# Kernel optimization log

Hardware: AMD Instinct MI355X
Metric: run time of the kernel (lower is better)

Reference implementation:

```python
import jax, jax.numpy as jnp
import numpy as np

N_NODES = 50000
N_EDGES = 800000


def setup_inputs() -> dict:
    key = jax.random.key(0)
    ks = jax.random.split(key, 9)
    d, h, hd = 128, 4, 32
    s = 1.0 / np.sqrt(d)
    return {
        "x": jax.random.normal(ks[0], (N_NODES, d), jnp.float32),
        "edge_index": jax.random.randint(ks[1], (2, N_EDGES), 0, N_NODES, jnp.int32),
        "W0": jax.random.normal(ks[2], (d, d), jnp.float32) * s,
        "att_l0": jax.random.normal(ks[3], (h, hd), jnp.float32) * s,
        "att_r0": jax.random.normal(ks[4], (h, hd), jnp.float32) * s,
        "b0": jnp.zeros((d,), jnp.float32),
        "W1": jax.random.normal(ks[5], (d, d), jnp.float32) * s,
        "att_l1": jax.random.normal(ks[6], (h, hd), jnp.float32) * s,
        "att_r1": jax.random.normal(ks[7], (h, hd), jnp.float32) * s,
        "b1": jnp.zeros((hd,), jnp.float32),
    }


def _gat_layer(x, src, dst, W, att_l, att_r, bias, concat):
    # x: [N, F_in]; W: [H*D, F_in] (torch Linear layout); att_*: [H, D]
    n = x.shape[0]
    h, d = att_l.shape
    hx = (x @ W.T).reshape(n, h, d)                     # [N,H,D]
    al = jnp.einsum('nhd,hd->nh', hx, att_l)            # [N,H]
    ar = jnp.einsum('nhd,hd->nh', hx, att_r)
    att = al[src] + ar[dst]                             # [E,H]
    att = jax.nn.leaky_relu(att, negative_slope=0.2)
    # segment softmax over destination nodes
    m = jax.ops.segment_max(att, dst, num_segments=n)   # [N,H]
    att = jnp.exp(att - m[dst])
    ssum = jax.ops.segment_sum(att, dst, num_segments=n)
    att = att / (ssum[dst] + 1e-9)                      # [E,H]
    msgs = att[:, :, None] * hx[src]                    # [E,H,D]
    out = jax.ops.segment_sum(msgs, dst, num_segments=n)  # [N,H,D]
    if concat:
        out = out.reshape(n, h * d)
    else:
        out = out.mean(axis=1)
    return out + bias


def reference(x, edge_index, W0, att_l0, att_r0, b0, W1, att_l1, att_r1, b1):
    src, dst = edge_index[0], edge_index[1]
    x = _gat_layer(x, src, dst, W0, att_l0, att_r0, b0, concat=True)
    x = jax.nn.relu(x)  # dropout is identity in eval mode
    x = _gat_layer(x, src, dst, W1, att_l1, att_r1, b1, concat=False)
    return x
```

## Files before the change

### kernel.cpp

```cpp
#include <hip/hip_runtime.h>
#include <hip/hip_bf16.h>

#define H 4
#define D 32
#define F 128
#define MAXDEG 64
#define PF 8
#define NBUCK 256
#define BUCKW 196
#define NABLK 128
#define SEGCAP 64
#define GB    1563
#define HXP   136
#define SIS   68

typedef __attribute__((ext_vector_type(8))) short bf16x8;
typedef __attribute__((ext_vector_type(4))) float f32x4;

__device__ __forceinline__ short f2bf(float v) {
    __hip_bfloat16 h = __float2bfloat16(v);
    return *reinterpret_cast<short*>(&h);
}
__device__ __forceinline__ float bf2f(short s) {
    __hip_bfloat16 h = *reinterpret_cast<__hip_bfloat16*>(&s);
    return __bfloat162float(h);
}

__device__ __forceinline__
void wconv_part(int part8, const float* __restrict__ W0, short* __restrict__ W0hi,
                short* __restrict__ W0lo, const float* __restrict__ W1,
                short* __restrict__ W1hi, short* __restrict__ W1lo) {
    const int tid = threadIdx.x;
    const float* W  = (part8 < 4) ? W0 : W1;
    short* Whi = (part8 < 4) ? W0hi : W1hi;
    short* Wlo = (part8 < 4) ? W0lo : W1lo;
    const int part = part8 & 3;
    const int base = part * (F * F / 4);
    for (int i = base + tid * 4; i < base + F * F / 4; i += 1024) {
        float4 v = *reinterpret_cast<const float4*>(W + i);
        float vv[4] = {v.x, v.y, v.z, v.w};
        short hs[4], ls[4];
#pragma unroll
        for (int j = 0; j < 4; ++j) {
            hs[j] = f2bf(vv[j]);
            ls[j] = f2bf(vv[j] - bf2f(hs[j]));
        }
        *reinterpret_cast<short4*>(Whi + i) = make_short4(hs[0], hs[1], hs[2], hs[3]);
        *reinterpret_cast<short4*>(Wlo + i) = make_short4(ls[0], ls[1], ls[2], ls[3]);
    }
}

__device__ __forceinline__
void bucketA_body(int abid, const int* __restrict__ ei, int E,
                  int* __restrict__ cntmat, unsigned int* __restrict__ buf) {
    __shared__ int lcnt[NBUCK];
    const int tid = threadIdx.x;
    lcnt[tid] = 0;
    __syncthreads();
    const int per = ((E / NABLK) + 3) & ~3;
    const int e0 = abid * per;
    const int e1 = min(e0 + per, E);
    for (int e = e0 + 4 * tid; e < e1; e += 1024) {
        int4 dv = *reinterpret_cast<const int4*>(ei + E + e);
        atomicAdd(&lcnt[dv.x / BUCKW], 1);
        atomicAdd(&lcnt[dv.y / BUCKW], 1);
        atomicAdd(&lcnt[dv.z / BUCKW], 1);
        atomicAdd(&lcnt[dv.w / BUCKW], 1);
    }
    __syncthreads();
    cntmat[abid * NBUCK + tid] = min(lcnt[tid], SEGCAP);
    lcnt[tid] = 0;
    __syncthreads();
    for (int e = e0 + 4 * tid; e < e1; e += 1024) {
        int4 sv = *reinterpret_cast<const int4*>(ei + e);
        int4 dv = *reinterpret_cast<const int4*>(ei + E + e);
        int ss[4] = {sv.x, sv.y, sv.z, sv.w};
        int dd[4] = {dv.x, dv.y, dv.z, dv.w};
#pragma unroll
        for (int j = 0; j < 4; ++j) {
            int b = dd[j] / BUCKW;
            int pos = atomicAdd(&lcnt[b], 1);
            if (pos < SEGCAP)
                buf[((size_t)b * NABLK + abid) * SEGCAP + pos] =
                    (unsigned)ss[j] | ((unsigned)(dd[j] - b * BUCKW) << 16);
        }
    }
}

__global__ __launch_bounds__(256)
void k_init(const int* __restrict__ ei, int E, int* __restrict__ cntmat,
            unsigned int* __restrict__ buf,
            const float* __restrict__ W0, short* __restrict__ W0hi,
            short* __restrict__ W0lo, const float* __restrict__ W1,
            short* __restrict__ W1hi, short* __restrict__ W1lo) {
    const int bid = blockIdx.x;
    if (bid < NABLK)
        bucketA_body(bid, ei, E, cntmat, buf);
    else
        wconv_part(bid - NABLK, W0, W0hi, W0lo, W1, W1hi, W1lo);
}

__device__ __forceinline__
void bucketB_body(int b, const unsigned int* __restrict__ buf,
                  const int* __restrict__ cntmat, int* __restrict__ deg,
                  unsigned short* __restrict__ ssrc2u, int N,
                  int* cnt, int* scnt, unsigned short* slots) {
    const int tid = threadIdx.x;
    if (tid < BUCKW) cnt[tid] = 0;
    if (tid < NABLK) scnt[tid] = cntmat[tid * NBUCK + b];
    __syncthreads();
    const int a    = tid & (NABLK - 1);
    const int half = tid >> 7;
    const int mm   = scnt[a];
    const unsigned int* seg = buf + ((size_t)b * NABLK + a) * SEGCAP;
    for (int c = half * 4; c < mm; c += 8) {
        uint4 r = *reinterpret_cast<const uint4*>(seg + c);
        unsigned rr[4] = {r.x, r.y, r.z, r.w};
#pragma unroll
        for (int j = 0; j < 4; ++j) {
            if (c + j < mm) {
                int src  = rr[j] & 0xffff;
                int ldst = rr[j] >> 16;
                int slot = atomicAdd(&cnt[ldst], 1);
                if (slot < MAXDEG)
                    slots[ldst * MAXDEG + slot] = (unsigned short)src;
            }
        }
    }
    __syncthreads();
    uint4* dst = reinterpret_cast<uint4*>(ssrc2u + (size_t)b * BUCKW * MAXDEG);
    const uint4* s4 = reinterpret_cast<const uint4*>(slots);
    for (int i = tid; i < BUCKW * MAXDEG / 8; i += 256)
        dst[i] = s4[i];
    if (tid < BUCKW) {
        int node = b * BUCKW + tid;
        if (node < N) deg[node] = cnt[tid];
    }
}

__device__ __forceinline__
void bsetup_pre(const short* __restrict__ Whi, const short* __restrict__ Wlo,
                int wave, int m, int q8, bf16x8 Bhi[2][4], bf16x8 Blo[2][4]) {
#pragma unroll
    for (int j = 0; j < 2; ++j) {
        const int fout = wave * 32 + j * 16 + m;
#pragma unroll
        for (int kc = 0; kc < 4; ++kc) {
            Bhi[j][kc] = *reinterpret_cast<const bf16x8*>(Whi + (size_t)fout * F + kc * 32 + q8);
            Blo[j][kc] = *reinterpret_cast<const bf16x8*>(Wlo + (size_t)fout * F + kc * 32 + q8);
        }
    }
}

__device__ __forceinline__
void loadA_f32(const float* __restrict__ X, int node0, int m, int q8, float4 r[8]) {
    const float* xp = X + (size_t)(node0 + m) * F + q8;
#pragma unroll
    for (int kc = 0; kc < 4; ++kc) {
        r[2 * kc]     = *reinterpret_cast<const float4*>(xp + kc * 32);
        r[2 * kc + 1] = *reinterpret_cast<const float4*>(xp + kc * 32 + 4);
    }
}

__device__ __forceinline__
void splitA(const float4 r[8], bf16x8 Ahi[4], bf16x8 Alo[4]) {
#pragma unroll
    for (int kc = 0; kc < 4; ++kc) {
        float xv[8] = {r[2 * kc].x, r[2 * kc].y, r[2 * kc].z, r[2 * kc].w,
                       r[2 * kc + 1].x, r[2 * kc + 1].y, r[2 * kc + 1].z, r[2 * kc + 1].w};
#pragma unroll
        for (int t2 = 0; t2 < 8; ++t2) {
            short hh = f2bf(xv[t2]);
            Ahi[kc][t2] = hh;
            Alo[kc][t2] = f2bf(xv[t2] - bf2f(hh));
        }
    }
}

__device__ __forceinline__
void mfma_epi(int tile, const bf16x8 Ahi[4], const bf16x8 Alo[4],
              const bf16x8 Bhi[2][4], const bf16x8 Blo[2][4],
              float alw0, float alw16, float arw0, float arw16,
              short* hxs, float* __restrict__ AL,
              float* __restrict__ AR, int wave, int m, int q) {
    const int node0 = tile * 16;
    f32x4 acc0 = {0.f, 0.f, 0.f, 0.f};
    f32x4 acc1 = {0.f, 0.f, 0.f, 0.f};
#pragma unroll
    for (int kc = 0; kc < 4; ++kc) {
        acc0 = __builtin_amdgcn_mfma_f32_16x16x32_bf16(Ahi[kc], Bhi[0][kc], acc0, 0, 0, 0);
        acc1 = __builtin_amdgcn_mfma_f32_16x16x32_bf16(Ahi[kc], Bhi[1][kc], acc1, 0, 0, 0);
        acc0 = __builtin_amdgcn_mfma_f32_16x16x32_bf16(Ahi[kc], Blo[0][kc], acc0, 0, 0, 0);
        acc1 = __builtin_amdgcn_mfma_f32_16x16x32_bf16(Ahi[kc], Blo[1][kc], acc1, 0, 0, 0);
        acc0 = __builtin_amdgcn_mfma_f32_16x16x32_bf16(Alo[kc], Bhi[0][kc], acc0, 0, 0, 0);
        acc1 = __builtin_amdgcn_mfma_f32_16x16x32_bf16(Alo[kc], Bhi[1][kc], acc1, 0, 0, 0);
    }
    const int row0 = node0 + q * 4;
    const int col0 = wave * 32 + m;
#pragma unroll
    for (int r = 0; r < 4; ++r) {
        hxs[(q * 4 + r) * HXP + col0]      = f2bf(acc0[r]);
        hxs[(q * 4 + r) * HXP + col0 + 16] = f2bf(acc1[r]);
        float pal = acc0[r] * alw0 + acc1[r] * alw16;
        float par = acc0[r] * arw0 + acc1[r] * arw16;
#pragma unroll
        for (int o = 1; o < 16; o <<= 1) {
            pal += __shfl_xor(pal, o);
            par += __shfl_xor(par, o);
        }
        if (m == 0) {
            AL[(size_t)(row0 + r) * H + wave] = pal;
            AR[(size_t)(row0 + r) * H + wave] = par;
        }
    }
}

__device__ __forceinline__
void hxb_writeout(const short* hxs, int tile, __hip_bfloat16* __restrict__ HXB) {
    const int tid = threadIdx.x;
    const int row = tid >> 4;
    const int col = (tid & 15) * 8;
    uint4 v = *reinterpret_cast<const uint4*>(hxs + row * HXP + col);
    *reinterpret_cast<uint4*>(reinterpret_cast<short*>(HXB) +
                              (size_t)(tile * 16 + row) * F + col) = v;
}

__device__ __forceinline__
void gemm_pair_f32(int bid, const float* __restrict__ X,
                   const short* __restrict__ Whi, const short* __restrict__ Wlo,
                   const float* __restrict__ attl, const float* __restrict__ attr,
                   __hip_bfloat16* __restrict__ HXB, float* __restrict__ AL,
                   float* __restrict__ AR, int ntiles, short* hxs) {
    const int wave = threadIdx.x >> 6;
    const int lane = threadIdx.x & 63;
    const int m    = lane & 15;
    const int q    = lane >> 4;
    const int q8   = q * 8;
    bf16x8 Bhi[2][4], Blo[2][4];
    bsetup_pre(Whi, Wlo, wave, m, q8, Bhi, Blo);
    const float alw0  = attl[wave * 32 + m];
    const float alw16 = attl[wave * 32 + 16 + m];
    const float arw0  = attr[wave * 32 + m];
    const float arw16 = attr[wave * 32 + 16 + m];

    const int t0 = bid, t1 = bid + GB;
    const bool has1 = t1 < ntiles;
    float4 r0[8], r1[8];
    loadA_f32(X, t0 * 16, m, q8, r0);
    if (has1) loadA_f32(X, t1 * 16, m, q8, r1);
    bf16x8 Ahi[4], Alo[4];
    splitA(r0, Ahi, Alo);
    mfma_epi(t0, Ahi, Alo, Bhi, Blo, alw0, alw16, arw0, arw16, hxs, AL, AR, wave, m, q);
    if (has1) {
        splitA(r1, Ahi, Alo);
        mfma_epi(t1, Ahi, Alo, Bhi, Blo, alw0, alw16, arw0, arw16,
                 hxs + 16 * HXP, AL, AR, wave, m, q);
    }
    __syncthreads();
    hxb_writeout(hxs, t0, HXB);
    if (has1) hxb_writeout(hxs + 16 * HXP, t1, HXB);
}

__global__ __launch_bounds__(256)
void k_mid(const unsigned int* __restrict__ buf, const int* __restrict__ cntmat,
           int* __restrict__ deg, unsigned short* __restrict__ ssrc2u, int N,
           const float* __restrict__ X, const short* __restrict__ W0hi,
           const short* __restrict__ W0lo, const float* __restrict__ attl0,
           const float* __restrict__ attr0, __hip_bfloat16* __restrict__ HXB,
           float* __restrict__ AL, float* __restrict__ AR, int ntiles) {
    __shared__ union {
        struct {
            int cnt[BUCKW];
            int scnt[NABLK];
            unsigned short slots[BUCKW * MAXDEG];
        } bb;
        short hxs[2 * 16 * HXP];
    } sm;
    const int bid = blockIdx.x;
    if (bid < NBUCK)
        bucketB_body(bid, buf, cntmat, deg, ssrc2u, N,
                     sm.bb.cnt, sm.bb.scnt, sm.bb.slots);
    else
        gemm_pair_f32(bid - NBUCK, X, W0hi, W0lo, attl0, attr0, HXB, AL, AR,
                      ntiles, sm.hxs);
}

__device__ __forceinline__
int2 stage_idx16(int g, int lt, int n, const unsigned short* __restrict__ ssrc2u,
                 const int* __restrict__ deg, unsigned short* sidx) {
    const int cnt  = min(deg[n], MAXDEG);
    const int rcnt = (cnt + PF - 1) & ~(PF - 1);
    for (int t2 = lt; t2 < rcnt; t2 += 16)
        sidx[g * SIS + t2] =
            (t2 < cnt) ? ssrc2u[(size_t)n * MAXDEG + t2] : (unsigned short)0;
    __builtin_amdgcn_wave_barrier();
    return make_int2(cnt, rcnt);
}

__device__ __forceinline__
void gather16(int g, int lt, int cnt, int rcnt,
              const __hip_bfloat16* __restrict__ HXB,
              const float* __restrict__ AL, float ar_h,
              const unsigned short* sidx, float a[8], float& wsum) {
    const int h = lt >> 2;
    const unsigned short* hx = reinterpret_cast<const unsigned short*>(HXB);
    for (int base = 0; base < rcnt; base += PF) {
        uint4 v[PF];
        float alv[PF];
#pragma unroll
        for (int j = 0; j < PF; ++j) {
            int s = sidx[g * SIS + base + j];
            v[j]   = *reinterpret_cast<const uint4*>(hx + (size_t)s * F + 8 * lt);
            alv[j] = AL[s * H + h];
        }
#pragma unroll
        for (int j = 0; j < PF; ++j) {
            float t = alv[j] + ar_h;
            t = t > 0.f ? t : 0.2f * t;
            float w = (base + j < cnt) ? __expf(t) : 0.f;
            unsigned ww[4] = {v[j].x, v[j].y, v[j].z, v[j].w};
#pragma unroll
            for (int k = 0; k < 4; ++k) {
                a[2 * k]     += w * bf2f((short)(ww[k] & 0xffff));
                a[2 * k + 1] += w * bf2f((short)(ww[k] >> 16));
            }
            wsum += w;
        }
    }
}

__global__ __launch_bounds__(256)
void k_ag1(const unsigned short* __restrict__ ssrc2u, const int* __restrict__ deg,
           const float* __restrict__ AL0, const float* __restrict__ AR0,
           const __hip_bfloat16* __restrict__ HXB0, const float* __restrict__ b0,
           const short* __restrict__ W1hi, const short* __restrict__ W1lo,
           const float* __restrict__ attl1, const float* __restrict__ attr1,
           __hip_bfloat16* __restrict__ HXB1, float* __restrict__ AL1,
           float* __restrict__ AR1, int ntiles) {
    __shared__ union {
        unsigned short sidx[16 * SIS];
        short hxs[16 * HXP];
    } u;
    __shared__ short x1h[16 * HXP];
    __shared__ short x1l[16 * HXP];
    const int tid  = threadIdx.x;
    const int g    = tid >> 4;
    const int lt   = tid & 15;
    const int tile = blockIdx.x;

    {
        const int n = tile * 16 + g;
        const int h = lt >> 2;
        const float ar_h = AR0[(size_t)n * H + h];
        int2 cr = stage_idx16(g, lt, n, ssrc2u, deg, u.sidx);
        float a[8] = {0.f, 0.f, 0.f, 0.f, 0.f, 0.f, 0.f, 0.f};
        float ws = 0.f;
        gather16(g, lt, cr.x, cr.y, HXB0, AL0, ar_h, u.sidx, a, ws);
        float inv = 1.f / (ws + 1e-9f);
        const float4 b4a = *reinterpret_cast<const float4*>(b0 + 8 * lt);
        const float4 b4b = *reinterpret_cast<const float4*>(b0 + 8 * lt + 4);
        float bb[8] = {b4a.x, b4a.y, b4a.z, b4a.w, b4b.x, b4b.y, b4b.z, b4b.w};
        unsigned hw[4], lw[4];
#pragma unroll
        for (int k = 0; k < 4; ++k) {
            float o0 = fmaxf(a[2 * k] * inv + bb[2 * k], 0.f);
            float o1 = fmaxf(a[2 * k + 1] * inv + bb[2 * k + 1], 0.f);
            short h0 = f2bf(o0), h1 = f2bf(o1);
            short l0 = f2bf(o0 - bf2f(h0)), l1 = f2bf(o1 - bf2f(h1));
            hw[k] = (unsigned)(unsigned short)h0 | ((unsigned)(unsigned short)h1 << 16);
            lw[k] = (unsigned)(unsigned short)l0 | ((unsigned)(unsigned short)l1 << 16);
        }
        uint4 hv = {hw[0], hw[1], hw[2], hw[3]};
        uint4 lv = {lw[0], lw[1], lw[2], lw[3]};
        *reinterpret_cast<uint4*>(x1h + g * HXP + 8 * lt) = hv;
        *reinterpret_cast<uint4*>(x1l + g * HXP + 8 * lt) = lv;
    }
    __syncthreads();

    {
        const int wave = tid >> 6;
        const int lane = tid & 63;
        const int m    = lane & 15;
        const int q    = lane >> 4;
        const int q8   = q * 8;
        bf16x8 Bhi[2][4], Blo[2][4];
        bsetup_pre(W1hi, W1lo, wave, m, q8, Bhi, Blo);
        const float alw0  = attl1[wave * 32 + m];
        const float alw16 = attl1[wave * 32 + 16 + m];
        const float arw0  = attr1[wave * 32 + m];
        const float arw16 = attr1[wave * 32 + 16 + m];
        bf16x8 Ahi[4], Alo[4];
#pragma unroll
        for (int kc = 0; kc < 4; ++kc) {
            Ahi[kc] = *reinterpret_cast<const bf16x8*>(x1h + m * HXP + kc * 32 + q8);
            Alo[kc] = *reinterpret_cast<const bf16x8*>(x1l + m * HXP + kc * 32 + q8);
        }
        mfma_epi(tile, Ahi, Alo, Bhi, Blo, alw0, alw16, arw0, arw16,
                 u.hxs, AL1, AR1, wave, m, q);
    }
    __syncthreads();
    hxb_writeout(u.hxs, tile, HXB1);
}

__global__ __launch_bounds__(256)
void k_aggr1(const unsigned short* __restrict__ ssrc2u, const int* __restrict__ deg,
             const float* __restrict__ AL, const float* __restrict__ AR,
             const __hip_bfloat16* __restrict__ HXB, const float* __restrict__ bias,
             float* __restrict__ out, int N) {
    __shared__ unsigned short sidx[16 * SIS];
    const int tid = threadIdx.x;
    const int g   = tid >> 4;
    const int lt  = tid & 15;
    const int n   = blockIdx.x * 16 + g;
    const int h   = lt >> 2;
    const float ar_h = AR[(size_t)n * H + h];
    int2 cr = stage_idx16(g, lt, n, ssrc2u, deg, sidx);
    float a[8] = {0.f, 0.f, 0.f, 0.f, 0.f, 0.f, 0.f, 0.f};
    float ws = 0.f;
    gather16(g, lt, cr.x, cr.y, HXB, AL, ar_h, sidx, a, ws);
    float inv = 1.f / (ws + 1e-9f);
    float v[8];
#pragma unroll
    for (int k = 0; k < 8; ++k) {
        v[k] = a[k] * inv;
        v[k] += __shfl_xor(v[k], 4);
        v[k] += __shfl_xor(v[k], 8);
    }
    if (lt < 4) {
        const float4 b4a = *reinterpret_cast<const float4*>(bias + 8 * lt);
        const float4 b4b = *reinterpret_cast<const float4*>(bias + 8 * lt + 4);
        float4 o0, o1;
        o0.x = 0.25f * v[0] + b4a.x;
        o0.y = 0.25f * v[1] + b4a.y;
        o0.z = 0.25f * v[2] + b4a.z;
        o0.w = 0.25f * v[3] + b4a.w;
        o1.x = 0.25f * v[4] + b4b.x;
        o1.y = 0.25f * v[5] + b4b.y;
        o1.z = 0.25f * v[6] + b4b.z;
        o1.w = 0.25f * v[7] + b4b.w;
        *reinterpret_cast<float4*>(out + (size_t)n * D + 8 * lt)     = o0;
        *reinterpret_cast<float4*>(out + (size_t)n * D + 8 * lt + 4) = o1;
    }
}

extern "C" void kernel_launch(void* const* d_in, const int* in_sizes, int n_in,
                              void* d_out, int out_size, void* d_ws, size_t ws_size,
                              hipStream_t stream) {
    const float* x     = (const float*)d_in[0];
    const int*   ei    = (const int*)d_in[1];
    const float* W0    = (const float*)d_in[2];
    const float* attl0 = (const float*)d_in[3];
    const float* attr0 = (const float*)d_in[4];
    const float* b0    = (const float*)d_in[5];
    const float* W1    = (const float*)d_in[6];
    const float* attl1 = (const float*)d_in[7];
    const float* attr1 = (const float*)d_in[8];
    const float* b1    = (const float*)d_in[9];

    const int N = in_sizes[0] / F;
    const int E = in_sizes[1] / 2;
    const int ntiles = N / 16;

    char* p = (char*)d_ws;
    __hip_bfloat16* HXB0 = (__hip_bfloat16*)p; p += (size_t)N * F * 2;
    __hip_bfloat16* HXB1 = (__hip_bfloat16*)p; p += (size_t)N * F * 2;
    short* W0hi = (short*)p;                   p += (size_t)F * F * 2;
    short* W0lo = (short*)p;                   p += (size_t)F * F * 2;
    short* W1hi = (short*)p;                   p += (size_t)F * F * 2;
    short* W1lo = (short*)p;                   p += (size_t)F * F * 2;
    float* AL0  = (float*)p;                   p += (size_t)N * H * 4;
    float* AR0  = (float*)p;                   p += (size_t)N * H * 4;
    float* AL1  = (float*)p;                   p += (size_t)N * H * 4;
    float* AR1  = (float*)p;                   p += (size_t)N * H * 4;
    unsigned short* ssrc2u = (unsigned short*)p;
    p += (size_t)NBUCK * BUCKW * MAXDEG * 2;
    int* deg = (int*)p;                        p += (size_t)N * 4;
    unsigned int* buf = (unsigned int*)p;      p += (size_t)NBUCK * NABLK * SEGCAP * 4;
    int* cntmat = (int*)p;

    k_init<<<NABLK + 8, 256, 0, stream>>>(ei, E, cntmat, buf,
                                          W0, W0hi, W0lo, W1, W1hi, W1lo);

    k_mid<<<NBUCK + GB, 256, 0, stream>>>(buf, cntmat, deg, ssrc2u, N,
                                          x, W0hi, W0lo, attl0, attr0,
                                          HXB0, AL0, AR0, ntiles);

    k_ag1<<<ntiles, 256, 0, stream>>>(ssrc2u, deg, AL0, AR0, HXB0, b0,
                                      W1hi, W1lo, attl1, attr1,
                                      HXB1, AL1, AR1, ntiles);

    k_aggr1<<<ntiles, 256, 0, stream>>>(ssrc2u, deg, AL1, AR1, HXB1, b1,
                                        (float*)d_out, N);
}
```

Measured before the change: 204.0 us.

## Sort nodes by degree within buckets to balance layer-1 aggregation tiles

Each bucket block now builds a degree histogram and a per-bucket permutation that groups nodes of similar in-degree. The first aggregation-plus-GEMM kernel processes nodes in this permuted order, so the 16 node groups in a tile have similar trip counts and less warp divergence and tail imbalance. Results are scattered back to their original rows through the rowids indirection, with padding nodes masked out. This adds a scan step, a serial prefix sum on one thread per bucket, scattered output writes and extra tiles to cover the padded node range.

```diff
diff --git a/kernel.cpp b/kernel.cpp
--- a/kernel.cpp
+++ b/kernel.cpp
@@ -8,6 +8,7 @@
 #define PF 8
 #define NBUCK 256
 #define BUCKW 196
+#define NPAD  (NBUCK * BUCKW)
 #define NABLK 128
 #define SEGCAP 64
 #define GB    1563
@@ -103,11 +104,12 @@
 __device__ __forceinline__
 void bucketB_body(int b, const unsigned int* __restrict__ buf,
                   const int* __restrict__ cntmat, int* __restrict__ deg,
-                  unsigned short* __restrict__ ssrc2u, int N,
-                  int* cnt, int* scnt, unsigned short* slots) {
+                  unsigned short* __restrict__ ssrc2u, int* __restrict__ perm,
+                  int N, int* cnt, int* scnt, int* dh, unsigned short* slots) {
     const int tid = threadIdx.x;
     if (tid < BUCKW) cnt[tid] = 0;
     if (tid < NABLK) scnt[tid] = cntmat[tid * NBUCK + b];
+    if (tid <= MAXDEG) dh[tid] = 0;
     __syncthreads();
     const int a    = tid & (NABLK - 1);
     const int half = tid >> 7;
@@ -132,9 +134,22 @@
     const uint4* s4 = reinterpret_cast<const uint4*>(slots);
     for (int i = tid; i < BUCKW * MAXDEG / 8; i += 256)
         dst[i] = s4[i];
+    int d = 0;
     if (tid < BUCKW) {
         int node = b * BUCKW + tid;
+        d = min(cnt[tid], MAXDEG);
         if (node < N) deg[node] = cnt[tid];
+        atomicAdd(&dh[d], 1);
+    }
+    __syncthreads();
+    if (tid == 0) {
+        int acc = 0;
+        for (int i = 0; i <= MAXDEG; ++i) { int c = dh[i]; dh[i] = acc; acc += c; }
+    }
+    __syncthreads();
+    if (tid < BUCKW) {
+        int r = atomicAdd(&dh[d], 1);
+        perm[b * BUCKW + r] = b * BUCKW + tid;
     }
 }
 
@@ -178,12 +193,12 @@
 }
 
 __device__ __forceinline__
-void mfma_epi(int tile, const bf16x8 Ahi[4], const bf16x8 Alo[4],
+void mfma_epi(int node0, const int* rowids, int Nlim,
+              const bf16x8 Ahi[4], const bf16x8 Alo[4],
               const bf16x8 Bhi[2][4], const bf16x8 Blo[2][4],
               float alw0, float alw16, float arw0, float arw16,
               short* hxs, float* __restrict__ AL,
               float* __restrict__ AR, int wave, int m, int q) {
-    const int node0 = tile * 16;
     f32x4 acc0 = {0.f, 0.f, 0.f, 0.f};
     f32x4 acc1 = {0.f, 0.f, 0.f, 0.f};
 #pragma unroll
@@ -195,7 +210,6 @@
         acc0 = __builtin_amdgcn_mfma_f32_16x16x32_bf16(Alo[kc], Bhi[0][kc], acc0, 0, 0, 0);
         acc1 = __builtin_amdgcn_mfma_f32_16x16x32_bf16(Alo[kc], Bhi[1][kc], acc1, 0, 0, 0);
     }
-    const int row0 = node0 + q * 4;
     const int col0 = wave * 32 + m;
 #pragma unroll
     for (int r = 0; r < 4; ++r) {
@@ -209,20 +223,27 @@
             par += __shfl_xor(par, o);
         }
         if (m == 0) {
-            AL[(size_t)(row0 + r) * H + wave] = pal;
-            AR[(size_t)(row0 + r) * H + wave] = par;
-        }
-    }
-}
-
-__device__ __forceinline__
-void hxb_writeout(const short* hxs, int tile, __hip_bfloat16* __restrict__ HXB) {
+            int rid = rowids ? rowids[q * 4 + r] : (node0 + q * 4 + r);
+            if (rid < Nlim) {
+                AL[(size_t)rid * H + wave] = pal;
+                AR[(size_t)rid * H + wave] = par;
+            }
+        }
+    }
+}
+
+__device__ __forceinline__
+void hxb_writeout(const short* hxs, int node0, const int* rowids, int Nlim,
+                  __hip_bfloat16* __restrict__ HXB) {
     const int tid = threadIdx.x;
     const int row = tid >> 4;
     const int col = (tid & 15) * 8;
-    uint4 v = *reinterpret_cast<const uint4*>(hxs + row * HXP + col);
-    *reinterpret_cast<uint4*>(reinterpret_cast<short*>(HXB) +
-                              (size_t)(tile * 16 + row) * F + col) = v;
+    int node = rowids ? rowids[row] : (node0 + row);
+    if (node < Nlim) {
+        uint4 v = *reinterpret_cast<const uint4*>(hxs + row * HXP + col);
+        *reinterpret_cast<uint4*>(reinterpret_cast<short*>(HXB) +
+                                  (size_t)node * F + col) = v;
+    }
 }
 
 __device__ __forceinline__
@@ -250,20 +271,22 @@
     if (has1) loadA_f32(X, t1 * 16, m, q8, r1);
     bf16x8 Ahi[4], Alo[4];
     splitA(r0, Ahi, Alo);
-    mfma_epi(t0, Ahi, Alo, Bhi, Blo, alw0, alw16, arw0, arw16, hxs, AL, AR, wave, m, q);
+    mfma_epi(t0 * 16, nullptr, 1 << 30, Ahi, Alo, Bhi, Blo,
+             alw0, alw16, arw0, arw16, hxs, AL, AR, wave, m, q);
     if (has1) {
         splitA(r1, Ahi, Alo);
-        mfma_epi(t1, Ahi, Alo, Bhi, Blo, alw0, alw16, arw0, arw16,
-                 hxs + 16 * HXP, AL, AR, wave, m, q);
-    }
-    __syncthreads();
-    hxb_writeout(hxs, t0, HXB);
-    if (has1) hxb_writeout(hxs + 16 * HXP, t1, HXB);
+        mfma_epi(t1 * 16, nullptr, 1 << 30, Ahi, Alo, Bhi, Blo,
+                 alw0, alw16, arw0, arw16, hxs + 16 * HXP, AL, AR, wave, m, q);
+    }
+    __syncthreads();
+    hxb_writeout(hxs, t0 * 16, nullptr, 1 << 30, HXB);
+    if (has1) hxb_writeout(hxs + 16 * HXP, t1 * 16, nullptr, 1 << 30, HXB);
 }
 
 __global__ __launch_bounds__(256)
 void k_mid(const unsigned int* __restrict__ buf, const int* __restrict__ cntmat,
-           int* __restrict__ deg, unsigned short* __restrict__ ssrc2u, int N,
+           int* __restrict__ deg, unsigned short* __restrict__ ssrc2u,
+           int* __restrict__ perm, int N,
            const float* __restrict__ X, const short* __restrict__ W0hi,
            const short* __restrict__ W0lo, const float* __restrict__ attl0,
            const float* __restrict__ attr0, __hip_bfloat16* __restrict__ HXB,
@@ -272,23 +295,25 @@
         struct {
             int cnt[BUCKW];
             int scnt[NABLK];
+            int dh[MAXDEG + 1];
             unsigned short slots[BUCKW * MAXDEG];
         } bb;
         short hxs[2 * 16 * HXP];
     } sm;
     const int bid = blockIdx.x;
     if (bid < NBUCK)
-        bucketB_body(bid, buf, cntmat, deg, ssrc2u, N,
-                     sm.bb.cnt, sm.bb.scnt, sm.bb.slots);
+        bucketB_body(bid, buf, cntmat, deg, ssrc2u, perm, N,
+                     sm.bb.cnt, sm.bb.scnt, sm.bb.dh, sm.bb.slots);
     else
         gemm_pair_f32(bid - NBUCK, X, W0hi, W0lo, attl0, attr0, HXB, AL, AR,
                       ntiles, sm.hxs);
 }
 
 __device__ __forceinline__
-int2 stage_idx16(int g, int lt, int n, const unsigned short* __restrict__ ssrc2u,
+int2 stage_idx16(int g, int lt, int n, int N,
+                 const unsigned short* __restrict__ ssrc2u,
                  const int* __restrict__ deg, unsigned short* sidx) {
-    const int cnt  = min(deg[n], MAXDEG);
+    const int cnt  = (n < N) ? min(deg[n], MAXDEG) : 0;
     const int rcnt = (cnt + PF - 1) & ~(PF - 1);
     for (int t2 = lt; t2 < rcnt; t2 += 16)
         sidx[g * SIS + t2] =
@@ -331,28 +356,32 @@
 
 __global__ __launch_bounds__(256)
 void k_ag1(const unsigned short* __restrict__ ssrc2u, const int* __restrict__ deg,
+           const int* __restrict__ perm,
            const float* __restrict__ AL0, const float* __restrict__ AR0,
            const __hip_bfloat16* __restrict__ HXB0, const float* __restrict__ b0,
            const short* __restrict__ W1hi, const short* __restrict__ W1lo,
            const float* __restrict__ attl1, const float* __restrict__ attr1,
            __hip_bfloat16* __restrict__ HXB1, float* __restrict__ AL1,
-           float* __restrict__ AR1, int ntiles) {
+           float* __restrict__ AR1, int N) {
     __shared__ union {
         unsigned short sidx[16 * SIS];
         short hxs[16 * HXP];
     } u;
     __shared__ short x1h[16 * HXP];
     __shared__ short x1l[16 * HXP];
+    __shared__ int   rowids[16];
     const int tid  = threadIdx.x;
     const int g    = tid >> 4;
     const int lt   = tid & 15;
     const int tile = blockIdx.x;
 
+    if (tid < 16) rowids[tid] = perm[tile * 16 + tid];
+
     {
-        const int n = tile * 16 + g;
+        const int n = perm[tile * 16 + g];
         const int h = lt >> 2;
-        const float ar_h = AR0[(size_t)n * H + h];
-        int2 cr = stage_idx16(g, lt, n, ssrc2u, deg, u.sidx);
+        const float ar_h = (n < N) ? AR0[(size_t)n * H + h] : 0.f;
+        int2 cr = stage_idx16(g, lt, n, N, ssrc2u, deg, u.sidx);
         float a[8] = {0.f, 0.f, 0.f, 0.f, 0.f, 0.f, 0.f, 0.f};
         float ws = 0.f;
         gather16(g, lt, cr.x, cr.y, HXB0, AL0, ar_h, u.sidx, a, ws);
@@ -395,11 +424,11 @@
             Ahi[kc] = *reinterpret_cast<const bf16x8*>(x1h + m * HXP + kc * 32 + q8);
             Alo[kc] = *reinterpret_cast<const bf16x8*>(x1l + m * HXP + kc * 32 + q8);
         }
-        mfma_epi(tile, Ahi, Alo, Bhi, Blo, alw0, alw16, arw0, arw16,
+        mfma_epi(0, rowids, N, Ahi, Alo, Bhi, Blo, alw0, alw16, arw0, arw16,
                  u.hxs, AL1, AR1, wave, m, q);
     }
     __syncthreads();
-    hxb_writeout(u.hxs, tile, HXB1);
+    hxb_writeout(u.hxs, 0, rowids, N, HXB1);
 }
 
 __global__ __launch_bounds__(256)
@@ -414,7 +443,7 @@
     const int n   = blockIdx.x * 16 + g;
     const int h   = lt >> 2;
     const float ar_h = AR[(size_t)n * H + h];
-    int2 cr = stage_idx16(g, lt, n, ssrc2u, deg, sidx);
+    int2 cr = stage_idx16(g, lt, n, N, ssrc2u, deg, sidx);
     float a[8] = {0.f, 0.f, 0.f, 0.f, 0.f, 0.f, 0.f, 0.f};
     float ws = 0.f;
     gather16(g, lt, cr.x, cr.y, HXB, AL, ar_h, sidx, a, ws);
@@ -473,21 +502,22 @@
     float* AL1  = (float*)p;                   p += (size_t)N * H * 4;
     float* AR1  = (float*)p;                   p += (size_t)N * H * 4;
     unsigned short* ssrc2u = (unsigned short*)p;
-    p += (size_t)NBUCK * BUCKW * MAXDEG * 2;
+    p += (size_t)NPAD * MAXDEG * 2;
     int* deg = (int*)p;                        p += (size_t)N * 4;
+    int* perm = (int*)p;                       p += (size_t)NPAD * 4;
     unsigned int* buf = (unsigned int*)p;      p += (size_t)NBUCK * NABLK * SEGCAP * 4;
     int* cntmat = (int*)p;
 
     k_init<<<NABLK + 8, 256, 0, stream>>>(ei, E, cntmat, buf,
                                           W0, W0hi, W0lo, W1, W1hi, W1lo);
 
-    k_mid<<<NBUCK + GB, 256, 0, stream>>>(buf, cntmat, deg, ssrc2u, N,
+    k_mid<<<NBUCK + GB, 256, 0, stream>>>(buf, cntmat, deg, ssrc2u, perm, N,
                                           x, W0hi, W0lo, attl0, attr0,
                                           HXB0, AL0, AR0, ntiles);
 
-    k_ag1<<<ntiles, 256, 0, stream>>>(ssrc2u, deg, AL0, AR0, HXB0, b0,
-                                      W1hi, W1lo, attl1, attr1,
-                                      HXB1, AL1, AR1, ntiles);
+    k_ag1<<<NPAD / 16, 256, 0, stream>>>(ssrc2u, deg, perm, AL0, AR0, HXB0, b0,
+                                         W1hi, W1lo, attl1, attr1,
+                                         HXB1, AL1, AR1, N);
 
     k_aggr1<<<ntiles, 256, 0, stream>>>(ssrc2u, deg, AL1, AR1, HXB1, b1,
                                         (float*)d_out, N);
```

Measured after the change: 205.9 us. Within noise of the previous version (+0.9%).
